# Kernel tuning notes

Measured on AMD Instinct MI355X. Metric: run time of the kernel, lower is better.

The kernel has to match this reference:

```python
import jax, jax.numpy as jnp
import numpy as np

B, T, D_IN = 32, 128, 32
H1, H, PEN = 1024, 2048, 1024  # linear1 out, GRU hidden, penultimate
C, P = 64, 4                   # cultivars, phenos


def setup_inputs() -> dict:
    key = jax.random.key(0)
    ks = jax.random.split(key, 22)
    s = 0.02
    inp = {}
    inp['x'] = jax.random.normal(ks[0], (B, T, D_IN), dtype=jnp.float32)
    inp['cultivar_label'] = jax.random.randint(ks[1], (B, 1), 0, C)
    inp['W1'] = jax.random.normal(ks[2], (H1, D_IN), dtype=jnp.float32) * s
    inp['b1'] = jnp.zeros((H1,), jnp.float32)
    inp['W2'] = jax.random.normal(ks[3], (H, H1), dtype=jnp.float32) * s
    inp['b2'] = jnp.zeros((H,), jnp.float32)
    # GRU weights, PyTorch layout: gates stacked (r,z,n) along dim 0
    inp['W_ih'] = jax.random.normal(ks[4], (3 * H, H), dtype=jnp.float32) * s
    inp['b_ih'] = jnp.zeros((3 * H,), jnp.float32)
    inp['W_hh'] = jax.random.normal(ks[5], (3 * H, H), dtype=jnp.float32) * s
    inp['b_hh'] = jnp.zeros((3 * H,), jnp.float32)
    inp['W3'] = jax.random.normal(ks[6], (PEN, H), dtype=jnp.float32) * s
    inp['b3'] = jnp.zeros((PEN,), jnp.float32)
    # per-cultivar expert heads (each a Linear(PEN, 1)) packed as tables
    inp['W4'] = jax.random.normal(ks[7], (C, PEN), dtype=jnp.float32) * s
    inp['b4'] = jnp.zeros((C,), jnp.float32)
    inp['W5'] = jax.random.normal(ks[8], (C, PEN), dtype=jnp.float32) * s
    inp['b5'] = jnp.zeros((C,), jnp.float32)
    inp['W6'] = jax.random.normal(ks[9], (C, PEN), dtype=jnp.float32) * s
    inp['b6'] = jnp.zeros((C,), jnp.float32)
    inp['Wp'] = jax.random.normal(ks[10], (P, C, PEN), dtype=jnp.float32) * s
    inp['bp'] = jnp.zeros((P, C), jnp.float32)
    return inp


def _gru(x_seq, W_ih, b_ih, W_hh, b_hh):
    # x_seq: [B,T,H]; PyTorch GRU gate order (r, z, n)
    Bd, Hd = x_seq.shape[0], W_hh.shape[1]
    xp = jnp.einsum('bth,gh->btg', x_seq, W_ih) + b_ih  # [B,T,3H]

    def step(h, xp_t):
        hp = h @ W_hh.T + b_hh
        xr, xz, xn = jnp.split(xp_t, 3, axis=-1)
        hr, hz, hn = jnp.split(hp, 3, axis=-1)
        r = jax.nn.sigmoid(xr + hr)
        z = jax.nn.sigmoid(xz + hz)
        n = jnp.tanh(xn + r * hn)
        h_new = (1.0 - z) * n + z * h
        return h_new, h_new

    h0 = jnp.zeros((Bd, Hd), x_seq.dtype)
    _, hs = jax.lax.scan(step, h0, jnp.swapaxes(xp, 0, 1))  # [T,B,H]
    return jnp.swapaxes(hs, 0, 1)  # [B,T,H]


def reference(x, cultivar_label, W1, b1, W2, b2, W_ih, b_ih, W_hh, b_hh,
              W3, b3, W4, b4, W5, b5, W6, b6, Wp, bp):
    out = jax.nn.relu(jnp.einsum('btd,hd->bth', x, W1) + b1)
    out = jax.nn.relu(jnp.einsum('bth,gh->btg', out, W2) + b2)
    out = _gru(out, W_ih, b_ih, W_hh, b_hh)
    out_s = jax.nn.relu(jnp.einsum('bth,ph->btp', out, W3) + b3)  # [B,T,PEN]
    labels = cultivar_label[:, 0]

    def head(W, b):  # gather expert row per sample -> [B,T,1]
        return (jnp.einsum('btd,bd->bt', out_s, W[labels]) + b[labels][:, None])[..., None]

    out_lt_10 = head(W4, b4)
    out_lt_50 = head(W5, b5)
    out_lt_90 = head(W6, b6)
    # pheno heads: Wp[:, labels] -> [P,B,PEN]
    out_ph = jax.nn.sigmoid(
        jnp.einsum('btd,pbd->pbt', out_s, Wp[:, labels]) + bp[:, labels][:, :, None]
    )[..., None]  # [P,B,T,1]
    return (out_lt_10, out_lt_50, out_lt_90, out_ph, 0)
```

## Files before the change

kernel.cpp:

```cpp
#include <hip/hip_runtime.h>
#include <hip/hip_bf16.h>
#include <math.h>


typedef __bf16 bf16_t;
typedef __bf16 bf16x4 __attribute__((ext_vector_type(4)));
typedef __bf16 bf16x8 __attribute__((ext_vector_type(8)));
typedef float  f32x4  __attribute__((ext_vector_type(4)));
typedef int    i32x4  __attribute__((ext_vector_type(4)));

static __device__ __forceinline__ void zero4(f32x4& v) {
  v[0] = 0.0f; v[1] = 0.0f; v[2] = 0.0f; v[3] = 0.0f;
}

template <typename T>
static __device__ __forceinline__ bf16x8 load8_as_bf16(const T* p);
template <>
__device__ __forceinline__ bf16x8 load8_as_bf16<bf16_t>(const bf16_t* p) {
  return *(const bf16x8*)p;
}
template <>
__device__ __forceinline__ bf16x8 load8_as_bf16<float>(const float* p) {
  bf16x8 v;
#pragma unroll
  for (int u = 0; u < 8; ++u) v[u] = (bf16_t)p[u];
  return v;
}

template <typename TA, typename TB>
__global__ __launch_bounds__(256) void gemm_bt(
    const TA* __restrict__ A, const TB* __restrict__ Bm,
    const float* __restrict__ bias, bf16_t* __restrict__ C,
    int M, int N, int K, int relu)
{
  __shared__ __align__(16) bf16_t As[128 * 32];
  __shared__ __align__(16) bf16_t Bs[128 * 32];

  const int tid  = threadIdx.x;
  const int lane = tid & 63;
  const int wave = tid >> 6;
  const int q    = lane >> 4;
  const int l15  = lane & 15;
  const int wr   = wave >> 1;
  const int wc   = wave & 1;
  const int m0   = blockIdx.y * 128;
  const int n0   = blockIdx.x * 128;

  f32x4 acc[4][4];
#pragma unroll
  for (int i = 0; i < 4; ++i)
#pragma unroll
    for (int j = 0; j < 4; ++j) zero4(acc[i][j]);

  const int se = wave * 512 + lane * 8;

  const int kt_count = K >> 5;
  for (int kt = 0; kt < kt_count; ++kt) {
    const int k0 = kt << 5;

    bf16x8 av[2], bv[2];
#pragma unroll
    for (int c = 0; c < 2; ++c) {
      const int e   = c * 2048 + se;
      const int row = e >> 5;
      const int col = e & 31;
      av[c] = load8_as_bf16<TA>(&A [(size_t)(m0 + row) * K + k0 + col]);
      bv[c] = load8_as_bf16<TB>(&Bm[(size_t)(n0 + row) * K + k0 + col]);
    }

    __syncthreads();
#pragma unroll
    for (int c = 0; c < 2; ++c) {
      *(bf16x8*)&As[c * 2048 + se] = av[c];
      *(bf16x8*)&Bs[c * 2048 + se] = bv[c];
    }
    __syncthreads();

    bf16x8 af[4], bfv[4];
#pragma unroll
    for (int i = 0; i < 4; ++i)
      af[i] = *(const bf16x8*)&As[(wr * 64 + i * 16 + l15) * 32 + q * 8];
#pragma unroll
    for (int j = 0; j < 4; ++j)
      bfv[j] = *(const bf16x8*)&Bs[(wc * 64 + j * 16 + l15) * 32 + q * 8];

#pragma unroll
    for (int i = 0; i < 4; ++i)
#pragma unroll
      for (int j = 0; j < 4; ++j)
        acc[i][j] = __builtin_amdgcn_mfma_f32_16x16x32_bf16(af[i], bfv[j], acc[i][j], 0, 0, 0);
  }

#pragma unroll
  for (int j = 0; j < 4; ++j) {
    const int n = n0 + wc * 64 + j * 16 + l15;
    const float bvl = bias[n];
#pragma unroll
    for (int i = 0; i < 4; ++i) {
      const int mbase = m0 + wr * 64 + i * 16 + q * 4;
#pragma unroll
      for (int r = 0; r < 4; ++r) {
        float v = acc[i][j][r] + bvl;
        if (relu) v = v > 0.0f ? v : 0.0f;
        C[(size_t)(mbase + r) * N + n] = (bf16_t)v;
      }
    }
  }
}

#define WROW 2056
#define NCOPY 8

__global__ __launch_bounds__(512, 2) void gru_persistent(
    const float* __restrict__ W_hh, const float* __restrict__ b_hh,
    const bf16_t* __restrict__ xp, bf16_t* __restrict__ hs,
    unsigned* __restrict__ arr)
{
  __shared__ __align__(16) bf16_t Ws[24 * WROW];
  __shared__ __align__(16) float hp_p[8][32][28];
  __shared__ __align__(16) unsigned short stage[32][8];

  const int tid  = threadIdx.x;
  const int lane = tid & 63;
  const int wave = tid >> 6;
  const int q    = lane >> 4;
  const int l15  = lane & 15;
  const int bid  = blockIdx.x;
  const int j0   = bid * 8;
  const int k0w  = wave * 256;

  for (int m = 0; m < 24; ++m) {
    const int gate = m >> 3;
    const float* src = W_hh + (size_t)(gate * 2048 + j0 + (m & 7)) * 2048;
    const int c = tid * 4;
    bf16x4 v;
#pragma unroll
    for (int u = 0; u < 4; ++u) v[u] = (bf16_t)src[c + u];
    *(bf16x4*)&Ws[m * WROW + c] = v;
  }

  const bool pw = tid < 256;
  const int b  = (tid >> 3) & 31;
  const int jj = tid & 7;
  const int jg = j0 + jj;
  float bh_r = 0.f, bh_z = 0.f, bh_n = 0.f;
  if (pw) {
    bh_r = b_hh[jg];
    bh_z = b_hh[2048 + jg];
    bh_n = b_hh[4096 + jg];
  }

  const bf16_t* arow0 = &Ws[(size_t)l15 * WROW + k0w];
  const bf16_t* arow1 = &Ws[(size_t)(16 + (l15 & 7)) * WROW + k0w];

  float hcur = 0.0f;

  float xr_c = 0.f, xz_c = 0.f, xn_c = 0.f;
  if (pw) {
    xr_c = (float)xp[(size_t)(b * 128 + 0) * 6144 + jg];
    xz_c = (float)xp[(size_t)(b * 128 + 0) * 6144 + 2048 + jg];
    xn_c = (float)xp[(size_t)(b * 128 + 0) * 6144 + 4096 + jg];
  }

  __syncthreads();

  for (int t = 0; t < 128; ++t) {
    if (t > 0) {
      const int c = bid & 7;
      const unsigned long long* f64p =
          (const unsigned long long*)(arr + ((size_t)(t - 1) * NCOPY + c) * 256)
          + wave * 16;
      const unsigned long long tgt = 0x0000000100000001ull;
      int guard = 0;
      for (;;) {
        unsigned long long v = tgt;
        if (lane < 16)
          v = __hip_atomic_load(f64p + lane, __ATOMIC_RELAXED,
                                __HIP_MEMORY_SCOPE_AGENT);
        if (__all(v == tgt)) break;
        __builtin_amdgcn_s_sleep(1);
        if (++guard > (1 << 20)) break;
      }

      bf16x8 bfr[2][8];
#pragma unroll
      for (int ct = 0; ct < 2; ++ct) {
        const bf16_t* bp_ = hs + ((size_t)(ct * 16 + l15) * 128 + (t - 1)) * 2048
                               + k0w + q * 8;
#pragma unroll
        for (int win = 0; win < 8; ++win)
          bfr[ct][win] = *(const bf16x8*)(bp_ + win * 32);
      }

      f32x4 acc[2][2];
#pragma unroll
      for (int rt = 0; rt < 2; ++rt)
#pragma unroll
        for (int ct = 0; ct < 2; ++ct) zero4(acc[rt][ct]);

#pragma unroll
      for (int win = 0; win < 8; ++win) {
        const bf16x8 a0 = *(const bf16x8*)(arow0 + win * 32 + q * 8);
        const bf16x8 a1 = *(const bf16x8*)(arow1 + win * 32 + q * 8);
        acc[0][0] = __builtin_amdgcn_mfma_f32_16x16x32_bf16(a0, bfr[0][win], acc[0][0], 0, 0, 0);
        acc[0][1] = __builtin_amdgcn_mfma_f32_16x16x32_bf16(a0, bfr[1][win], acc[0][1], 0, 0, 0);
        acc[1][0] = __builtin_amdgcn_mfma_f32_16x16x32_bf16(a1, bfr[0][win], acc[1][0], 0, 0, 0);
        acc[1][1] = __builtin_amdgcn_mfma_f32_16x16x32_bf16(a1, bfr[1][win], acc[1][1], 0, 0, 0);
      }

#pragma unroll
      for (int ct = 0; ct < 2; ++ct) {
        *(f32x4*)&hp_p[wave][ct * 16 + l15][q * 4] = acc[0][ct];
        if (q < 2)
          *(f32x4*)&hp_p[wave][ct * 16 + l15][16 + q * 4] = acc[1][ct];
      }
    }
    __syncthreads();

    float xr_n = 0.f, xz_n = 0.f, xn_n = 0.f;
    if (pw) {
      float pr = 0.0f, pz = 0.0f, pn = 0.0f;
      if (t > 0) {
#pragma unroll
        for (int w = 0; w < 8; ++w) {
          pr += hp_p[w][b][jj];
          pz += hp_p[w][b][8 + jj];
          pn += hp_p[w][b][16 + jj];
        }
      }
      const float r_ = 1.0f / (1.0f + __expf(-(xr_c + pr + bh_r)));
      const float z_ = 1.0f / (1.0f + __expf(-(xz_c + pz + bh_z)));
      const float aa = xn_c + r_ * (pn + bh_n);
      const float et = __expf(-2.0f * aa);
      const float n_ = (1.0f - et) / (1.0f + et);
      hcur = (1.0f - z_) * n_ + z_ * hcur;

      if (t < 127) {
        const int tn = t + 1;
        xr_n = (float)xp[(size_t)(b * 128 + tn) * 6144 + jg];
        xz_n = (float)xp[(size_t)(b * 128 + tn) * 6144 + 2048 + jg];
        xn_n = (float)xp[(size_t)(b * 128 + tn) * 6144 + 4096 + jg];
      }

      union { bf16_t h; unsigned short u; } cv; cv.h = (bf16_t)hcur;
      stage[b][jj] = cv.u;
    }
    __syncthreads();

    if (wave == 0 && lane < 32) {
      const i32x4 val = *(const i32x4*)&stage[lane][0];
      bf16_t* dst = hs + ((size_t)lane * 128 + t) * 2048 + j0;
      asm volatile("global_store_dwordx4 %0, %1, off sc0 sc1"
                   :: "v"(dst), "v"(val) : "memory");
    }
    if (t < 127) {
      if (wave == 0) {
        asm volatile("s_waitcnt vmcnt(0)" ::: "memory");
        if (lane < NCOPY)
          __hip_atomic_store(arr + ((size_t)t * NCOPY + lane) * 256 + bid, 1u,
                             __ATOMIC_RELAXED, __HIP_MEMORY_SCOPE_AGENT);
      }
      xr_c = xr_n; xz_c = xz_n; xn_c = xn_n;
    }
  }
}

__global__ __launch_bounds__(256) void heads_kernel(
    const bf16_t* __restrict__ out_s, const int* __restrict__ labels,
    const float* __restrict__ W4, const float* __restrict__ b4,
    const float* __restrict__ W5, const float* __restrict__ b5,
    const float* __restrict__ W6, const float* __restrict__ b6,
    const float* __restrict__ Wp, const float* __restrict__ bp,
    float* __restrict__ out)
{
  const int bt  = blockIdx.x;
  const int b   = bt >> 7;
  const int lab = labels[b];
  const bf16_t* os  = out_s + (size_t)bt * 1024;
  const float* w4  = W4 + (size_t)lab * 1024;
  const float* w5  = W5 + (size_t)lab * 1024;
  const float* w6  = W6 + (size_t)lab * 1024;
  const float* wp0 = Wp + (size_t)lab * 1024;

  float s[7] = {0, 0, 0, 0, 0, 0, 0};
  for (int d = threadIdx.x; d < 1024; d += 256) {
    const float v = (float)os[d];
    s[0] += v * w4[d];
    s[1] += v * w5[d];
    s[2] += v * w6[d];
    s[3] += v * wp0[d];
    s[4] += v * wp0[65536 + d];
    s[5] += v * wp0[131072 + d];
    s[6] += v * wp0[196608 + d];
  }
#pragma unroll
  for (int i = 0; i < 7; ++i)
    for (int off = 32; off > 0; off >>= 1)
      s[i] += __shfl_down(s[i], off, 64);

  __shared__ float red[4][7];
  const int lane = threadIdx.x & 63, wave = threadIdx.x >> 6;
  if (lane == 0)
    for (int i = 0; i < 7; ++i) red[wave][i] = s[i];
  __syncthreads();
  if (threadIdx.x == 0) {
    float tsum[7];
    for (int i = 0; i < 7; ++i)
      tsum[i] = red[0][i] + red[1][i] + red[2][i] + red[3][i];
    out[bt]        = tsum[0] + b4[lab];
    out[4096 + bt] = tsum[1] + b5[lab];
    out[8192 + bt] = tsum[2] + b6[lab];
#pragma unroll
    for (int p = 0; p < 4; ++p) {
      const float v = tsum[3 + p] + bp[p * 64 + lab];
      out[12288 + p * 4096 + bt] = 1.0f / (1.0f + __expf(-v));
    }
  }
}

extern "C" void kernel_launch(void* const* d_in, const int* in_sizes, int n_in,
                              void* d_out, int out_size, void* d_ws, size_t ws_size,
                              hipStream_t stream)
{
  const float* x     = (const float*)d_in[0];
  const int*   label = (const int*)d_in[1];
  const float* W1    = (const float*)d_in[2];
  const float* b1    = (const float*)d_in[3];
  const float* W2    = (const float*)d_in[4];
  const float* b2    = (const float*)d_in[5];
  const float* W_ih  = (const float*)d_in[6];
  const float* b_ih  = (const float*)d_in[7];
  const float* W_hh  = (const float*)d_in[8];
  const float* b_hh  = (const float*)d_in[9];
  const float* W3    = (const float*)d_in[10];
  const float* b3    = (const float*)d_in[11];
  const float* W4    = (const float*)d_in[12];
  const float* b4    = (const float*)d_in[13];
  const float* W5    = (const float*)d_in[14];
  const float* b5    = (const float*)d_in[15];
  const float* W6    = (const float*)d_in[16];
  const float* b6    = (const float*)d_in[17];
  const float* Wp    = (const float*)d_in[18];
  const float* bp    = (const float*)d_in[19];

  char* ws = (char*)d_ws;
  unsigned* arr = (unsigned*)ws;
  bf16_t* out1  = (bf16_t*)(ws + (24u << 20));
  bf16_t* out2  = (bf16_t*)(ws + (32u << 20));
  bf16_t* xp    = (bf16_t*)(ws + (48u << 20));
  bf16_t* hs    = (bf16_t*)(ws + (24u << 20));
  bf16_t* out_s = (bf16_t*)(ws + (40u << 20));
  float*  outp  = (float*)d_out;

  hipMemsetAsync(d_out, 0, (size_t)out_size * sizeof(float), stream);
  hipMemsetAsync(ws, 0, 1u << 20, stream);

  dim3 blk(256);
  gemm_bt<float, float><<<dim3(8, 32), blk, 0, stream>>>(x, W1, b1, out1, 4096, 1024, 32, 1);
  gemm_bt<bf16_t, float><<<dim3(16, 32), blk, 0, stream>>>(out1, W2, b2, out2, 4096, 2048, 1024, 1);
  gemm_bt<bf16_t, float><<<dim3(48, 32), blk, 0, stream>>>(out2, W_ih, b_ih, xp, 4096, 6144, 2048, 0);
  {
    void* gru_args[] = { (void*)&W_hh, (void*)&b_hh, (void*)&xp, (void*)&hs,
                         (void*)&arr };
    hipLaunchCooperativeKernel((void*)gru_persistent, dim3(256), dim3(512),
                               gru_args, 0, stream);
  }
  gemm_bt<bf16_t, float><<<dim3(8, 32), blk, 0, stream>>>(hs, W3, b3, out_s, 4096, 1024, 2048, 1);
  heads_kernel<<<dim3(4096), blk, 0, stream>>>(out_s, label, W4, b4, W5, b5, W6, b6, Wp, bp, outp);
}
```

Baseline: 1.338 ms.

## Fuse W3 projection into persistent GRU and use bf16 LDS-DMA GEMMs

The W3 output projection is folded into the persistent GRU kernel. Each block computes 4 output columns of out_s per step from the same h fragments it already loads, and handles the final timestep after a last grid-wide wait. The W2 and W_ih weights are converted to bf16 up front, and those GEMMs switch to a kernel that stages tiles with global_load_lds direct-to-LDS loads. The changes are meant to remove the separate W3 GEMM launch and to avoid converting fp32 weights inside the GEMM inner loops. In exchange the GRU step gets extra MFMA work and LDS use, and two conversion kernels are added.

```diff
diff --git a/kernel.cpp b/kernel.cpp
--- a/kernel.cpp
+++ b/kernel.cpp
@@ -8,6 +8,7 @@
 typedef __bf16 bf16x8 __attribute__((ext_vector_type(8)));
 typedef float  f32x4  __attribute__((ext_vector_type(4)));
 typedef int    i32x4  __attribute__((ext_vector_type(4)));
+typedef unsigned int u32;
 
 static __device__ __forceinline__ void zero4(f32x4& v) {
   v[0] = 0.0f; v[1] = 0.0f; v[2] = 0.0f; v[3] = 0.0f;
@@ -25,6 +26,25 @@
 #pragma unroll
   for (int u = 0; u < 8; ++u) v[u] = (bf16_t)p[u];
   return v;
+}
+
+static __device__ __forceinline__ void gload16(const bf16_t* g, bf16_t* l) {
+  __builtin_amdgcn_global_load_lds(
+      (const __attribute__((address_space(1))) u32*)g,
+      (__attribute__((address_space(3))) u32*)l, 16, 0, 0);
+}
+
+__global__ __launch_bounds__(256) void cvt_f32_bf16(
+    const float* __restrict__ s, bf16_t* __restrict__ d, int n8)
+{
+  const int i = blockIdx.x * 256 + threadIdx.x;
+  if (i < n8) {
+    const float* p = s + (size_t)i * 8;
+    bf16x8 v;
+#pragma unroll
+    for (int u = 0; u < 8; ++u) v[u] = (bf16_t)p[u];
+    *(bf16x8*)(d + (size_t)i * 8) = v;
+  }
 }
 
 template <typename TA, typename TB>
@@ -108,16 +128,95 @@
   }
 }
 
+__global__ __launch_bounds__(256) void gemm_lds(
+    const bf16_t* __restrict__ A, const bf16_t* __restrict__ Bm,
+    const float* __restrict__ bias, bf16_t* __restrict__ C,
+    int M, int N, int K, int relu)
+{
+  __shared__ __align__(16) bf16_t As[128 * 32];
+  __shared__ __align__(16) bf16_t Bs[128 * 32];
+
+  const int tid  = threadIdx.x;
+  const int lane = tid & 63;
+  const int wave = tid >> 6;
+  const int q    = lane >> 4;
+  const int l15  = lane & 15;
+  const int wr   = wave >> 1;
+  const int wc   = wave & 1;
+  const int m0   = blockIdx.y * 128;
+  const int n0   = blockIdx.x * 128;
+
+  f32x4 acc[4][4];
+#pragma unroll
+  for (int i = 0; i < 4; ++i)
+#pragma unroll
+    for (int j = 0; j < 4; ++j) zero4(acc[i][j]);
+
+  const int sew = wave * 512;
+  const int se  = sew + lane * 8;
+
+  const int kt_count = K >> 5;
+  for (int kt = 0; kt < kt_count; ++kt) {
+    const int k0 = kt << 5;
+
+    __syncthreads();
+#pragma unroll
+    for (int c = 0; c < 2; ++c) {
+      const int e   = c * 2048 + se;
+      const int row = e >> 5;
+      const int col = e & 31;
+      gload16(&A [(size_t)(m0 + row) * K + k0 + col], &As[c * 2048 + sew]);
+      gload16(&Bm[(size_t)(n0 + row) * K + k0 + col], &Bs[c * 2048 + sew]);
+    }
+    asm volatile("s_waitcnt vmcnt(0)" ::: "memory");
+    __syncthreads();
+
+    bf16x8 af[4], bfv[4];
+#pragma unroll
+    for (int i = 0; i < 4; ++i)
+      af[i] = *(const bf16x8*)&As[(wr * 64 + i * 16 + l15) * 32 + q * 8];
+#pragma unroll
+    for (int j = 0; j < 4; ++j)
+      bfv[j] = *(const bf16x8*)&Bs[(wc * 64 + j * 16 + l15) * 32 + q * 8];
+
+#pragma unroll
+    for (int i = 0; i < 4; ++i)
+#pragma unroll
+      for (int j = 0; j < 4; ++j)
+        acc[i][j] = __builtin_amdgcn_mfma_f32_16x16x32_bf16(af[i], bfv[j], acc[i][j], 0, 0, 0);
+  }
+
+#pragma unroll
+  for (int j = 0; j < 4; ++j) {
+    const int n = n0 + wc * 64 + j * 16 + l15;
+    const float bvl = bias[n];
+#pragma unroll
+    for (int i = 0; i < 4; ++i) {
+      const int mbase = m0 + wr * 64 + i * 16 + q * 4;
+#pragma unroll
+      for (int r = 0; r < 4; ++r) {
+        float v = acc[i][j][r] + bvl;
+        if (relu) v = v > 0.0f ? v : 0.0f;
+        C[(size_t)(mbase + r) * N + n] = (bf16_t)v;
+      }
+    }
+  }
+}
+
 #define WROW 2056
 #define NCOPY 8
 
 __global__ __launch_bounds__(512, 2) void gru_persistent(
     const float* __restrict__ W_hh, const float* __restrict__ b_hh,
     const bf16_t* __restrict__ xp, bf16_t* __restrict__ hs,
-    unsigned* __restrict__ arr)
+    unsigned* __restrict__ arr,
+    const float* __restrict__ W3, const float* __restrict__ b3,
+    bf16_t* __restrict__ out_s)
 {
   __shared__ __align__(16) bf16_t Ws[24 * WROW];
+  __shared__ __align__(16) bf16_t W3s[4 * WROW];
   __shared__ __align__(16) float hp_p[8][32][28];
+  __shared__ __align__(16) float hp3[8][32][8];
   __shared__ __align__(16) unsigned short stage[32][8];
 
   const int tid  = threadIdx.x;
@@ -127,6 +226,7 @@
   const int l15  = lane & 15;
   const int bid  = blockIdx.x;
   const int j0   = bid * 8;
+  const int j0s  = bid * 4;
   const int k0w  = wave * 256;
 
   for (int m = 0; m < 24; ++m) {
@@ -137,6 +237,14 @@
 #pragma unroll
     for (int u = 0; u < 4; ++u) v[u] = (bf16_t)src[c + u];
     *(bf16x4*)&Ws[m * WROW + c] = v;
+  }
+  for (int m = 0; m < 4; ++m) {
+    const float* src = W3 + (size_t)(j0s + m) * 2048;
+    const int c = tid * 4;
+    bf16x4 v;
+#pragma unroll
+    for (int u = 0; u < 4; ++u) v[u] = (bf16_t)src[c + u];
+    *(bf16x4*)&W3s[m * WROW + c] = v;
   }
 
   const bool pw = tid < 256;
@@ -149,9 +257,15 @@
     bh_z = b_hh[2048 + jg];
     bh_n = b_hh[4096 + jg];
   }
+  const bool sw = (tid >= 256) && (tid < 384);
+  const int b3t = (tid - 256) >> 2;
+  const int c3  = (tid - 256) & 3;
+  float b3v = 0.f;
+  if (sw) b3v = b3[j0s + c3];
 
   const bf16_t* arow0 = &Ws[(size_t)l15 * WROW + k0w];
   const bf16_t* arow1 = &Ws[(size_t)(16 + (l15 & 7)) * WROW + k0w];
+  const bf16_t* arow3 = &W3s[(size_t)(l15 & 3) * WROW + k0w];
 
   float hcur = 0.0f;
 
@@ -208,11 +322,24 @@
         acc[1][1] = __builtin_amdgcn_mfma_f32_16x16x32_bf16(a1, bfr[1][win], acc[1][1], 0, 0, 0);
       }
 
+      f32x4 acc3[2];
+      zero4(acc3[0]); zero4(acc3[1]);
+#pragma unroll
+      for (int win = 0; win < 8; ++win) {
+        const bf16x8 a3 = *(const bf16x8*)(arow3 + win * 32 + q * 8);
+        acc3[0] = __builtin_amdgcn_mfma_f32_16x16x32_bf16(a3, bfr[0][win], acc3[0], 0, 0, 0);
+        acc3[1] = __builtin_amdgcn_mfma_f32_16x16x32_bf16(a3, bfr[1][win], acc3[1], 0, 0, 0);
+      }
+
 #pragma unroll
       for (int ct = 0; ct < 2; ++ct) {
         *(f32x4*)&hp_p[wave][ct * 16 + l15][q * 4] = acc[0][ct];
         if (q < 2)
           *(f32x4*)&hp_p[wave][ct * 16 + l15][16 + q * 4] = acc[1][ct];
+      }
+      if (q == 0) {
+        *(f32x4*)&hp3[wave][l15][0]      = acc3[0];
+        *(f32x4*)&hp3[wave][16 + l15][0] = acc3[1];
       }
     }
     __syncthreads();
@@ -244,6 +371,13 @@
 
       union { bf16_t h; unsigned short u; } cv; cv.h = (bf16_t)hcur;
       stage[b][jj] = cv.u;
+    } else if (sw && t > 0) {
+      float s3 = 0.0f;
+#pragma unroll
+      for (int w = 0; w < 8; ++w) s3 += hp3[w][b3t][c3];
+      s3 += b3v;
+      if (s3 < 0.0f) s3 = 0.0f;
+      out_s[((size_t)b3t * 128 + (t - 1)) * 1024 + j0s + c3] = (bf16_t)s3;
     }
     __syncthreads();
 
@@ -253,14 +387,59 @@
       asm volatile("global_store_dwordx4 %0, %1, off sc0 sc1"
                    :: "v"(dst), "v"(val) : "memory");
     }
+    if (wave == 0) {
+      asm volatile("s_waitcnt vmcnt(0)" ::: "memory");
+      if (lane < NCOPY)
+        __hip_atomic_store(arr + ((size_t)t * NCOPY + lane) * 256 + bid, 1u,
+                           __ATOMIC_RELAXED, __HIP_MEMORY_SCOPE_AGENT);
+    }
     if (t < 127) {
-      if (wave == 0) {
-        asm volatile("s_waitcnt vmcnt(0)" ::: "memory");
-        if (lane < NCOPY)
-          __hip_atomic_store(arr + ((size_t)t * NCOPY + lane) * 256 + bid, 1u,
-                             __ATOMIC_RELAXED, __HIP_MEMORY_SCOPE_AGENT);
-      }
       xr_c = xr_n; xz_c = xz_n; xn_c = xn_n;
+    }
+  }
+
+  {
+    const int c = bid & 7;
+    const unsigned long long* f64p =
+        (const unsigned long long*)(arr + ((size_t)127 * NCOPY + c) * 256)
+        + wave * 16;
+    const unsigned long long tgt = 0x0000000100000001ull;
+    int guard = 0;
+    for (;;) {
+      unsigned long long v = tgt;
+      if (lane < 16)
+        v = __hip_atomic_load(f64p + lane, __ATOMIC_RELAXED,
+                              __HIP_MEMORY_SCOPE_AGENT);
+      if (__all(v == tgt)) break;
+      __builtin_amdgcn_s_sleep(1);
+      if (++guard > (1 << 20)) break;
+    }
+
+    f32x4 acc3[2];
+    zero4(acc3[0]); zero4(acc3[1]);
+#pragma unroll
+    for (int ct = 0; ct < 2; ++ct) {
+      const bf16_t* bp_ = hs + ((size_t)(ct * 16 + l15) * 128 + 127) * 2048
+                             + k0w + q * 8;
+#pragma unroll
+      for (int win = 0; win < 8; ++win) {
+        const bf16x8 bv = *(const bf16x8*)(bp_ + win * 32);
+        const bf16x8 a3 = *(const bf16x8*)(arow3 + win * 32 + q * 8);
+        acc3[ct] = __builtin_amdgcn_mfma_f32_16x16x32_bf16(a3, bv, acc3[ct], 0, 0, 0);
+      }
+    }
+    if (q == 0) {
+      *(f32x4*)&hp3[wave][l15][0]      = acc3[0];
+      *(f32x4*)&hp3[wave][16 + l15][0] = acc3[1];
+    }
+    __syncthreads();
+    if (sw) {
+      float s3 = 0.0f;
+#pragma unroll
+      for (int w = 0; w < 8; ++w) s3 += hp3[w][b3t][c3];
+      s3 += b3v;
+      if (s3 < 0.0f) s3 = 0.0f;
+      out_s[((size_t)b3t * 128 + 127) * 1024 + j0s + c3] = (bf16_t)s3;
     }
   }
 }
@@ -344,27 +523,30 @@
   const float* bp    = (const float*)d_in[19];
 
   char* ws = (char*)d_ws;
-  unsigned* arr = (unsigned*)ws;
-  bf16_t* out1  = (bf16_t*)(ws + (24u << 20));
-  bf16_t* out2  = (bf16_t*)(ws + (32u << 20));
-  bf16_t* xp    = (bf16_t*)(ws + (48u << 20));
-  bf16_t* hs    = (bf16_t*)(ws + (24u << 20));
-  bf16_t* out_s = (bf16_t*)(ws + (40u << 20));
+  bf16_t* W_ihb = (bf16_t*)(ws);
+  bf16_t* out2  = (bf16_t*)(ws + (24u << 20));
+  bf16_t* W2b   = (bf16_t*)(ws + (40u << 20));
+  bf16_t* out1  = (bf16_t*)(ws + (44u << 20));
+  bf16_t* xp    = (bf16_t*)(ws + (47u << 20));
+  bf16_t* hs    = (bf16_t*)(ws);
+  bf16_t* out_s = (bf16_t*)(ws + (16u << 20));
+  unsigned* arr = (unsigned*)(ws + (95u << 20));
   float*  outp  = (float*)d_out;
 
   hipMemsetAsync(d_out, 0, (size_t)out_size * sizeof(float), stream);
-  hipMemsetAsync(ws, 0, 1u << 20, stream);
+  hipMemsetAsync(arr, 0, 1u << 20, stream);
 
   dim3 blk(256);
+  cvt_f32_bf16<<<dim3(6144), blk, 0, stream>>>(W_ih, W_ihb, 1572864);
+  cvt_f32_bf16<<<dim3(1024), blk, 0, stream>>>(W2, W2b, 262144);
   gemm_bt<float, float><<<dim3(8, 32), blk, 0, stream>>>(x, W1, b1, out1, 4096, 1024, 32, 1);
-  gemm_bt<bf16_t, float><<<dim3(16, 32), blk, 0, stream>>>(out1, W2, b2, out2, 4096, 2048, 1024, 1);
-  gemm_bt<bf16_t, float><<<dim3(48, 32), blk, 0, stream>>>(out2, W_ih, b_ih, xp, 4096, 6144, 2048, 0);
+  gemm_lds<<<dim3(16, 32), blk, 0, stream>>>(out1, W2b, b2, out2, 4096, 2048, 1024, 1);
+  gemm_lds<<<dim3(48, 32), blk, 0, stream>>>(out2, W_ihb, b_ih, xp, 4096, 6144, 2048, 0);
   {
     void* gru_args[] = { (void*)&W_hh, (void*)&b_hh, (void*)&xp, (void*)&hs,
-                         (void*)&arr };
+                         (void*)&arr, (void*)&W3, (void*)&b3, (void*)&out_s };
     hipLaunchCooperativeKernel((void*)gru_persistent, dim3(256), dim3(512),
                                gru_args, 0, stream);
   }
-  gemm_bt<bf16_t, float><<<dim3(8, 32), blk, 0, stream>>>(hs, W3, b3, out_s, 4096, 1024, 2048, 1);
   heads_kernel<<<dim3(4096), blk, 0, stream>>>(out_s, label, W4, b4, W5, b5, W6, b6, Wp, bp, outp);
 }
```

Measured after the change: 1.274 ms. 4.8% less time.
